# Kernel optimization log

Hardware: AMD Instinct MI355X
Metric: run time of the kernel (lower is better)

Reference implementation:

```python
import jax, jax.numpy as jnp
import numpy as np

DIM = 256
HEADS = 4
DEPTH = DIM // HEADS
EXPAND = 4
EPS = 1e-3  # keras BatchNormalization default epsilon


def _bn(x, gamma, beta, mean, var):
    # inference-mode batch norm over last axis
    return gamma * (x - mean) * jax.lax.rsqrt(var + EPS) + beta


def setup_inputs() -> dict:
    key = jax.random.key(0)
    ks = jax.random.split(key, 12)
    B, S, D = 4, 2048, DIM
    H = D * EXPAND
    s = 1.0 / np.sqrt(D)
    inp = {
        "x": jax.random.normal(ks[0], (B, S, D), jnp.float32),
        "bn1_gamma": jnp.ones((D,), jnp.float32),
        "bn1_beta": jnp.zeros((D,), jnp.float32),
        "bn1_mean": jax.random.normal(ks[1], (D,), jnp.float32) * 0.1,
        "bn1_var": jnp.abs(jax.random.normal(ks[2], (D,), jnp.float32)) + 0.5,
        "wq": jax.random.normal(ks[3], (D, D), jnp.float32) * s,
        "bq": jnp.zeros((D,), jnp.float32),
        "wk": jax.random.normal(ks[4], (D, D), jnp.float32) * s,
        "bk": jnp.zeros((D,), jnp.float32),
        "wv": jax.random.normal(ks[5], (D, D), jnp.float32) * s,
        "bv": jnp.zeros((D,), jnp.float32),
        "wo": jax.random.normal(ks[6], (D, D), jnp.float32) * s,
        "bo": jnp.zeros((D,), jnp.float32),
        "bn2_gamma": jnp.ones((D,), jnp.float32),
        "bn2_beta": jnp.zeros((D,), jnp.float32),
        "bn2_mean": jax.random.normal(ks[7], (D,), jnp.float32) * 0.1,
        "bn2_var": jnp.abs(jax.random.normal(ks[8], (D,), jnp.float32)) + 0.5,
        "w1": jax.random.normal(ks[9], (D, H), jnp.float32) * s,
        "w2": jax.random.normal(ks[10], (H, D), jnp.float32) * (1.0 / np.sqrt(H)),
    }
    return inp


def reference(x, bn1_gamma, bn1_beta, bn1_mean, bn1_var,
              wq, bq, wk, bk, wv, bv, wo, bo,
              bn2_gamma, bn2_beta, bn2_mean, bn2_var, w1, w2):
    B, S, D = x.shape
    h = _bn(x, bn1_gamma, bn1_beta, bn1_mean, bn1_var)
    # project and split heads -> [B, H, S, depth]
    def heads(t):
        return t.reshape(B, S, HEADS, DEPTH).transpose(0, 2, 1, 3)
    q = heads(h @ wq + bq)
    k = heads(h @ wk + bk)
    v = heads(h @ wv + bv)
    scores = jnp.einsum("bhqd,bhkd->bhqk", q, k) / jnp.sqrt(jnp.float32(DEPTH))
    attn = jax.nn.softmax(scores, axis=-1)
    ctx = jnp.einsum("bhqk,bhkd->bhqd", attn, v)
    ctx = ctx.transpose(0, 2, 1, 3).reshape(B, S, D)
    attn_out = ctx @ wo + bo
    x1 = attn_out + x  # residual (dropout = identity at inference)
    h2 = _bn(x1, bn2_gamma, bn2_beta, bn2_mean, bn2_var)
    m = jax.nn.gelu(h2 @ w1, approximate=False) @ w2
    return m + x1
```

## Files before the change

### kernel.cpp

```cpp
#include <hip/hip_runtime.h>

typedef unsigned short u16;
typedef unsigned int u32;
typedef short short8 __attribute__((ext_vector_type(8)));
typedef short short4v __attribute__((ext_vector_type(4)));
typedef float f32x4 __attribute__((ext_vector_type(4)));

#define EPS 1e-3f
#define C1F 0.18033688011112042f

#if defined(__HIP_DEVICE_COMPILE__)
#define MFMA16(a, b, c) __builtin_amdgcn_mfma_f32_16x16x16bf16_1k(a, b, c, 0, 0, 0)
#else
#define MFMA16(a, b, c) (c)
#endif

static __device__ __forceinline__ u16 f2bf(float f) {
    u32 u = __float_as_uint(f);
    u += 0x7fffu + ((u >> 16) & 1u);
    return (u16)(u >> 16);
}
static __device__ __forceinline__ float bf2f(u16 v) {
    u32 u = (u32)v << 16;
    return __uint_as_float(u);
}
static __device__ __forceinline__ u32 pack_bf2(float a, float b) {
    u32 ua = __float_as_uint(a) + 0x8000u;
    u32 ub = __float_as_uint(b) + 0x8000u;
    return __builtin_amdgcn_perm(ub, ua, 0x07060302u);
}
static __device__ __forceinline__ void async_cp16(const void* g, void* l) {
    __builtin_amdgcn_global_load_lds(
        (const __attribute__((address_space(1))) unsigned int*)g,
        (__attribute__((address_space(3))) unsigned int*)l, 16, 0, 0);
}

__global__ void prep_kernel(const float* __restrict__ wq, const float* __restrict__ wk,
                            const float* __restrict__ wv, const float* __restrict__ wo,
                            const float* __restrict__ w1, const float* __restrict__ w2,
                            const float* __restrict__ bq, const float* __restrict__ bk,
                            const float* __restrict__ bv,
                            const float* __restrict__ g1, const float* __restrict__ b1,
                            const float* __restrict__ m1, const float* __restrict__ v1,
                            const float* __restrict__ g2, const float* __restrict__ b2,
                            const float* __restrict__ m2, const float* __restrict__ v2,
                            u16* __restrict__ wqkvT, u16* __restrict__ woT,
                            u16* __restrict__ w1T, u16* __restrict__ w2T,
                            float* __restrict__ bqkv,
                            float* __restrict__ bn1sc, float* __restrict__ bn1sh,
                            float* __restrict__ bn2sc, float* __restrict__ bn2sh) {
    int idx = blockIdx.x * 256 + threadIdx.x;
    if (idx < 196608) {
        int sec = idx >> 16;
        int i = idx & 65535;
        int k = i >> 8, n = i & 255;
        const float* w = sec == 0 ? wq : (sec == 1 ? wk : wv);
        float v = w[i];
        if (sec == 1) v *= C1F;
        wqkvT[(sec * 256 + n) * 256 + k] = f2bf(v);
    } else if (idx < 262144) {
        int i = idx - 196608; int k = i >> 8, n = i & 255;
        woT[n * 256 + k] = f2bf(wo[i]);
    } else if (idx < 524288) {
        int i = idx - 262144; int k = i >> 10, n = i & 1023;
        w1T[n * 256 + k] = f2bf(w1[i]);
    } else if (idx < 786432) {
        int i = idx - 524288; int k = i >> 8, n = i & 255;
        w2T[n * 1024 + k] = f2bf(w2[i]);
    } else if (idx < 787200) {
        int i = idx - 786432;
        bqkv[i] = (i < 256) ? bq[i] : (i < 512 ? bk[i - 256] * C1F : bv[i - 512]);
    } else if (idx < 787456) {
        int i = idx - 787200;
        float sc = g1[i] * rsqrtf(v1[i] + EPS);
        bn1sc[i] = sc; bn1sh[i] = b1[i] - m1[i] * sc;
    } else if (idx < 787712) {
        int i = idx - 787456;
        float sc = g2[i] * rsqrtf(v2[i] + EPS);
        bn2sc[i] = sc; bn2sh[i] = b2[i] - m2[i] * sc;
    }
}

__global__ void bn1_kernel(const float* __restrict__ x, const float* __restrict__ sc,
                           const float* __restrict__ sh, u16* __restrict__ h) {
    int idx = blockIdx.x * 256 + threadIdx.x;
    int base = idx * 4;
    int c = base & 255;
    float4 xv = *(const float4*)(x + base);
    float4 s4 = *(const float4*)(sc + c);
    float4 h4 = *(const float4*)(sh + c);
    ushort4 pk;
    pk.x = f2bf(fmaf(xv.x, s4.x, h4.x));
    pk.y = f2bf(fmaf(xv.y, s4.y, h4.y));
    pk.z = f2bf(fmaf(xv.z, s4.z, h4.z));
    pk.w = f2bf(fmaf(xv.w, s4.w, h4.w));
    *(ushort4*)(h + base) = pk;
}

template <int EPI>
__global__ __launch_bounds__(256) void gemm64(
        const u16* __restrict__ A, const u16* __restrict__ Bt,
        int M, int N, int K,
        const float* __restrict__ bias, const float* __restrict__ resid,
        float* __restrict__ out_f32, u16* __restrict__ out_bf,
        u16* __restrict__ out_vt,
        const float* __restrict__ b2sc, const float* __restrict__ b2sh) {
    __shared__ u16 abuf[2][4096];
    __shared__ u16 bbuf[2][4096];
    const int t = threadIdx.x;
    const int w = t >> 6, lane = t & 63;
    const int l = lane & 15, Q = lane >> 4;
    const int m0 = blockIdx.x * 64;
    const int n0 = blockIdx.y * 64;

    f32x4 acc[4];
#pragma unroll
    for (int nt = 0; nt < 4; ++nt) acc[nt] = (f32x4){0.f, 0.f, 0.f, 0.f};

    auto stage = [&](int k0, int b) {
#pragma unroll
        for (int j = 0; j < 2; ++j) {
            int idx = j * 256 + t;
            int r = idx >> 3, c8 = idx & 7;
            int sc = c8 ^ (r & 7);
            async_cp16(A + (size_t)(m0 + r) * K + k0 + sc * 8, abuf[b] + idx * 8);
        }
#pragma unroll
        for (int j = 0; j < 2; ++j) {
            int idx = j * 256 + t;
            int r = idx >> 3, c8 = idx & 7;
            int sc = c8 ^ (r & 7);
            async_cp16(Bt + (size_t)(n0 + r) * K + k0 + sc * 8, bbuf[b] + idx * 8);
        }
    };

    const int nit = K >> 6;
    stage(0, 0);
    for (int i = 0; i < nit; ++i) {
        __syncthreads();
        if (i + 1 < nit) stage((i + 1) << 6, (i + 1) & 1);
        const u16* ab = abuf[i & 1];
        const u16* bb = bbuf[i & 1];
#pragma unroll
        for (int kd = 0; kd < 2; ++kd) {
            int ar = w * 16 + l;
            short8 afr = *(const short8*)(ab + ar * 64 + (((kd * 4 + Q) ^ (ar & 7))) * 8);
#pragma unroll
            for (int nt = 0; nt < 4; ++nt) {
                int r = nt * 16 + l;
                short8 bfr = *(const short8*)(bb + r * 64 + (((kd * 4 + Q) ^ (r & 7))) * 8);
                acc[nt] = __builtin_amdgcn_mfma_f32_16x16x32_bf16(afr, bfr, acc[nt], 0, 0, 0);
            }
        }
    }

#pragma unroll
    for (int nt = 0; nt < 4; ++nt) {
        int col = n0 + nt * 16 + l;
        int row0 = m0 + w * 16 + Q * 4;
        if (EPI == 0) {
            float b = bias[col];
            if (col < 512) {
#pragma unroll
                for (int r = 0; r < 4; ++r)
                    out_bf[(size_t)(row0 + r) * 512 + col] = f2bf(acc[nt][r] + b);
            } else {
                ushort4 pk;
                pk.x = f2bf(acc[nt][0] + b);
                pk.y = f2bf(acc[nt][1] + b);
                pk.z = f2bf(acc[nt][2] + b);
                pk.w = f2bf(acc[nt][3] + b);
                *(ushort4*)(out_vt + (size_t)(col - 512) * 8192 + row0) = pk;
            }
        } else {
#pragma unroll
            for (int r = 0; r < 4; ++r) {
                int row = row0 + r;
                float val = acc[nt][r];
                size_t oidx = (size_t)row * N + col;
                if (EPI == 1) {
                    val += bias[col] + resid[oidx];
                    out_f32[oidx] = val;
                    out_bf[oidx] = f2bf(fmaf(val, b2sc[col], b2sh[col]));
                } else if (EPI == 2) {
                    float gl = 0.5f * val * (1.f + erff(val * 0.70710678118654752f));
                    out_bf[oidx] = f2bf(gl);
                } else {
                    out_f32[oidx] = val + resid[oidx];
                }
            }
        }
    }
}

static __device__ __forceinline__ void stage_tiles8(const u16* kglob, const u16* vglob,
                                                    u16* kdst, u16* vdst,
                                                    int w, int lane, int kt) {
    const int wp = w & 3;
#pragma unroll
    for (int j = 0; j < 2; ++j) {
        int cw = (wp * 2 + j) * 64 + lane;
        int r = cw >> 3;
        int c = (cw & 7) ^ (r & 7);
        if (w < 4)
            async_cp16(kglob + ((size_t)(kt * 64 + r)) * 512 + c * 8, kdst + (wp * 2 + j) * 512);
        else
            async_cp16(vglob + ((size_t)r) * 8192 + kt * 64 + c * 8, vdst + (wp * 2 + j) * 512);
    }
}

__global__ __launch_bounds__(512) void attn_kernel(const u16* __restrict__ qk,
                                                   const u16* __restrict__ vT,
                                                   u16* __restrict__ opart,
                                                   float* __restrict__ lpart) {
    __shared__ u16 kbuf[2][4096];
    __shared__ u16 vbuf[2][4096];
    const int t = threadIdx.x;
    const int w = t >> 6, lane = t & 63;
    const int l = lane & 15, Q = lane >> 4;
    const int qt = blockIdx.x;
    const int bh = blockIdx.y;
    const int sp = blockIdx.z;
    const int bb = bh >> 2, hd = bh & 3;
    const size_t rowbase = (size_t)bb * 2048;
    const int q0 = qt * 256 + w * 32;

    short8 qf[2][2];
#pragma unroll
    for (int qg = 0; qg < 2; ++qg)
#pragma unroll
        for (int kd = 0; kd < 2; ++kd)
            qf[qg][kd] = *(const short8*)(qk + (rowbase + q0 + qg * 16 + l) * 512
                                          + hd * 64 + kd * 32 + Q * 8);

    f32x4 o[2][4];
#pragma unroll
    for (int qg = 0; qg < 2; ++qg)
#pragma unroll
        for (int dt = 0; dt < 4; ++dt) o[qg][dt] = (f32x4){0.f, 0.f, 0.f, 0.f};
    float lacc[2] = {0.f, 0.f};

    const u16* kglob = qk + (rowbase + sp * 256) * 512 + 256 + hd * 64;
    const u16* vglob = vT + ((size_t)(hd * 64)) * 8192 + rowbase + sp * 256;

    stage_tiles8(kglob, vglob, kbuf[0], vbuf[0], w, lane, 0);

    for (int kt = 0; kt < 4; ++kt) {
        __syncthreads();
        if (kt < 3)
            stage_tiles8(kglob, vglob, kbuf[(kt + 1) & 1], vbuf[(kt + 1) & 1], w, lane, kt + 1);
        const u16* kb = kbuf[kt & 1];
        const u16* vb = vbuf[kt & 1];

        union { u32 u[2]; short4v s4; } pf[2][4];
#pragma unroll
        for (int st = 0; st < 4; ++st) {
            int r = st * 16 + l;
            short8 kf0 = *(const short8*)(kb + r * 64 + ((Q) ^ (r & 7)) * 8);
            short8 kf1 = *(const short8*)(kb + r * 64 + ((4 + Q) ^ (r & 7)) * 8);
#pragma unroll
            for (int qg = 0; qg < 2; ++qg) {
                f32x4 s = (f32x4){0.f, 0.f, 0.f, 0.f};
                s = __builtin_amdgcn_mfma_f32_16x16x32_bf16(kf0, qf[qg][0], s, 0, 0, 0);
                s = __builtin_amdgcn_mfma_f32_16x16x32_bf16(kf1, qf[qg][1], s, 0, 0, 0);
                float p0 = exp2f(fminf(s[0], 100.f));
                float p1 = exp2f(fminf(s[1], 100.f));
                float p2 = exp2f(fminf(s[2], 100.f));
                float p3 = exp2f(fminf(s[3], 100.f));
                lacc[qg] += (p0 + p1) + (p2 + p3);
                pf[qg][st].u[0] = pack_bf2(p0, p1);
                pf[qg][st].u[1] = pack_bf2(p2, p3);
            }
        }

#pragma unroll
        for (int c = 0; c < 4; ++c) {
#pragma unroll
            for (int dt = 0; dt < 4; ++dt) {
                int r = dt * 16 + l;
                int slot = (2 * c + (Q >> 1)) ^ (r & 7);
                short4v vf = *(const short4v*)(vb + r * 64 + slot * 8 + (Q & 1) * 4);
                o[0][dt] = MFMA16(vf, pf[0][c].s4, o[0][dt]);
                o[1][dt] = MFMA16(vf, pf[1][c].s4, o[1][dt]);
            }
        }
    }

#pragma unroll
    for (int qg = 0; qg < 2; ++qg) {
        float v = lacc[qg];
        v += __shfl_xor(v, 16);
        v += __shfl_xor(v, 32);
        lacc[qg] = v;
    }
    u16* ob = opart + (((size_t)sp * 16 + bh) * 2048 + q0) * 64;
#pragma unroll
    for (int qg = 0; qg < 2; ++qg)
#pragma unroll
        for (int dt = 0; dt < 4; ++dt) {
            ushort4 pk;
            pk.x = f2bf(o[qg][dt][0]);
            pk.y = f2bf(o[qg][dt][1]);
            pk.z = f2bf(o[qg][dt][2]);
            pk.w = f2bf(o[qg][dt][3]);
            *(ushort4*)(ob + (size_t)(qg * 16 + l) * 64 + dt * 16 + Q * 4) = pk;
        }
    if (Q == 0) {
        size_t lb = ((size_t)sp * 16 + bh) * 2048 + q0;
        lpart[lb + l] = lacc[0];
        lpart[lb + 16 + l] = lacc[1];
    }
}

__global__ void combine_kernel(const u16* __restrict__ opart,
                               const float* __restrict__ lpart,
                               u16* __restrict__ ctx) {
    int idx = blockIdx.x * 256 + threadIdx.x;
    int e = idx * 4;
    int row = e >> 8, col = e & 255;
    int b = row >> 11, s = row & 2047, h = col >> 6, d = col & 63;
    float a0 = 0.f, a1 = 0.f, a2 = 0.f, a3 = 0.f, lsum = 0.f;
#pragma unroll
    for (int sp = 0; sp < 8; ++sp) {
        size_t pb = (((size_t)sp * 16 + b * 4 + h) * 2048 + s) * 64 + d;
        ushort4 ov = *(const ushort4*)(opart + pb);
        a0 += bf2f(ov.x); a1 += bf2f(ov.y); a2 += bf2f(ov.z); a3 += bf2f(ov.w);
        lsum += lpart[((size_t)sp * 16 + b * 4 + h) * 2048 + s];
    }
    float li = 1.0f / lsum;
    ushort4 pk;
    pk.x = f2bf(a0 * li);
    pk.y = f2bf(a1 * li);
    pk.z = f2bf(a2 * li);
    pk.w = f2bf(a3 * li);
    *(ushort4*)(ctx + e) = pk;
}

extern "C" void kernel_launch(void* const* d_in, const int* in_sizes, int n_in,
                              void* d_out, int out_size, void* d_ws, size_t ws_size,
                              hipStream_t stream) {
    (void)in_sizes; (void)n_in; (void)out_size; (void)ws_size;
    const float* x  = (const float*)d_in[0];
    const float* g1 = (const float*)d_in[1];
    const float* b1 = (const float*)d_in[2];
    const float* m1 = (const float*)d_in[3];
    const float* v1 = (const float*)d_in[4];
    const float* wq = (const float*)d_in[5];
    const float* bq = (const float*)d_in[6];
    const float* wk = (const float*)d_in[7];
    const float* bk = (const float*)d_in[8];
    const float* wv = (const float*)d_in[9];
    const float* bv = (const float*)d_in[10];
    const float* wo = (const float*)d_in[11];
    const float* bo = (const float*)d_in[12];
    const float* g2 = (const float*)d_in[13];
    const float* b2 = (const float*)d_in[14];
    const float* m2 = (const float*)d_in[15];
    const float* v2 = (const float*)d_in[16];
    const float* w1 = (const float*)d_in[17];
    const float* w2 = (const float*)d_in[18];

    char* ws = (char*)d_ws;
    u16*   qkb    = (u16*)(ws + (0ull << 20));
    u16*   vTb    = (u16*)(ws + (8ull << 20));
    u16*   h_buf  = (u16*)(ws + (12ull << 20));
    u16*   ctx    = (u16*)(ws + (16ull << 20));
    float* x1     = (float*)(ws + (20ull << 20));
    u16*   h2     = (u16*)(ws + (28ull << 20));
    u16*   gbuf   = (u16*)(ws + (32ull << 20));
    u16*   opart  = (u16*)(ws + (48ull << 20));
    float* lpart  = (float*)(ws + (80ull << 20));
    u16*   wqkvT  = (u16*)(ws + (81ull << 20));
    u16*   woT    = (u16*)(ws + (82ull << 20));
    u16*   w1T    = (u16*)(ws + (83ull << 20));
    u16*   w2T    = (u16*)(ws + (84ull << 20));
    float* bqkv   = (float*)(ws + (85ull << 20));
    float* bn1sc  = (float*)(ws + (85ull << 20) + 4096);
    float* bn1sh  = (float*)(ws + (85ull << 20) + 8192);
    float* bn2sc  = (float*)(ws + (85ull << 20) + 12288);
    float* bn2sh  = (float*)(ws + (85ull << 20) + 16384);
    float* out    = (float*)d_out;

    prep_kernel<<<3077, 256, 0, stream>>>(wq, wk, wv, wo, w1, w2, bq, bk, bv,
                                          g1, b1, m1, v1, g2, b2, m2, v2,
                                          wqkvT, woT, w1T, w2T, bqkv,
                                          bn1sc, bn1sh, bn2sc, bn2sh);
    bn1_kernel<<<2048, 256, 0, stream>>>(x, bn1sc, bn1sh, h_buf);
    gemm64<0><<<dim3(128, 12), 256, 0, stream>>>(
        h_buf, wqkvT, 8192, 768, 256, bqkv, nullptr, nullptr, qkb, vTb, nullptr, nullptr);
    attn_kernel<<<dim3(8, 16, 8), 512, 0, stream>>>(qkb, vTb, opart, lpart);
    combine_kernel<<<2048, 256, 0, stream>>>(opart, lpart, ctx);
    gemm64<1><<<dim3(128, 4), 256, 0, stream>>>(
        ctx, woT, 8192, 256, 256, bo, x, x1, h2, nullptr, bn2sc, bn2sh);
    gemm64<2><<<dim3(128, 16), 256, 0, stream>>>(
        h2, w1T, 8192, 1024, 256, nullptr, nullptr, nullptr, gbuf, nullptr, nullptr, nullptr);
    gemm64<3><<<dim3(128, 4), 256, 0, stream>>>(
        gbuf, w2T, 8192, 256, 1024, nullptr, x1, out, nullptr, nullptr, nullptr, nullptr);
}
```

Before: 199.7 us.

## Fuse FFN GEMMs, merge BN1 into prep, reshape attention blocks

```diff
diff --git a/kernel.cpp b/kernel.cpp
--- a/kernel.cpp
+++ b/kernel.cpp
@@ -24,10 +24,8 @@
     u32 u = (u32)v << 16;
     return __uint_as_float(u);
 }
-static __device__ __forceinline__ u32 pack_bf2(float a, float b) {
-    u32 ua = __float_as_uint(a) + 0x8000u;
-    u32 ub = __float_as_uint(b) + 0x8000u;
-    return __builtin_amdgcn_perm(ub, ua, 0x07060302u);
+static __device__ __forceinline__ u32 pack_bf2_trunc(float a, float b) {
+    return __builtin_amdgcn_perm(__float_as_uint(b), __float_as_uint(a), 0x07060302u);
 }
 static __device__ __forceinline__ void async_cp16(const void* g, void* l) {
     __builtin_amdgcn_global_load_lds(
@@ -35,7 +33,8 @@
         (__attribute__((address_space(3))) unsigned int*)l, 16, 0, 0);
 }
 
-__global__ void prep_kernel(const float* __restrict__ wq, const float* __restrict__ wk,
+__global__ void prep_bn1_kernel(const float* __restrict__ x,
+                            const float* __restrict__ wq, const float* __restrict__ wk,
                             const float* __restrict__ wv, const float* __restrict__ wo,
                             const float* __restrict__ w1, const float* __restrict__ w2,
                             const float* __restrict__ bq, const float* __restrict__ bk,
@@ -44,12 +43,33 @@
                             const float* __restrict__ m1, const float* __restrict__ v1,
                             const float* __restrict__ g2, const float* __restrict__ b2,
                             const float* __restrict__ m2, const float* __restrict__ v2,
+                            u16* __restrict__ h,
                             u16* __restrict__ wqkvT, u16* __restrict__ woT,
                             u16* __restrict__ w1T, u16* __restrict__ w2T,
                             float* __restrict__ bqkv,
                             float* __restrict__ bn1sc, float* __restrict__ bn1sh,
                             float* __restrict__ bn2sc, float* __restrict__ bn2sh) {
-    int idx = blockIdx.x * 256 + threadIdx.x;
+    int bid = blockIdx.x;
+    if (bid < 2048) {
+        int idx = bid * 256 + threadIdx.x;
+        int base = idx * 4;
+        int c = base & 255;
+        float4 xv = *(const float4*)(x + base);
+        ushort4 pk;
+        {
+            float sc0 = g1[c] * rsqrtf(v1[c] + EPS);
+            pk.x = f2bf(fmaf(xv.x, sc0, b1[c] - m1[c] * sc0));
+            float sc1 = g1[c+1] * rsqrtf(v1[c+1] + EPS);
+            pk.y = f2bf(fmaf(xv.y, sc1, b1[c+1] - m1[c+1] * sc1));
+            float sc2 = g1[c+2] * rsqrtf(v1[c+2] + EPS);
+            pk.z = f2bf(fmaf(xv.z, sc2, b1[c+2] - m1[c+2] * sc2));
+            float sc3 = g1[c+3] * rsqrtf(v1[c+3] + EPS);
+            pk.w = f2bf(fmaf(xv.w, sc3, b1[c+3] - m1[c+3] * sc3));
+        }
+        *(ushort4*)(h + base) = pk;
+        return;
+    }
+    int idx = (bid - 2048) * 256 + threadIdx.x;
     if (idx < 196608) {
         int sec = idx >> 16;
         int i = idx & 65535;
@@ -81,22 +101,6 @@
     }
 }
 
-__global__ void bn1_kernel(const float* __restrict__ x, const float* __restrict__ sc,
-                           const float* __restrict__ sh, u16* __restrict__ h) {
-    int idx = blockIdx.x * 256 + threadIdx.x;
-    int base = idx * 4;
-    int c = base & 255;
-    float4 xv = *(const float4*)(x + base);
-    float4 s4 = *(const float4*)(sc + c);
-    float4 h4 = *(const float4*)(sh + c);
-    ushort4 pk;
-    pk.x = f2bf(fmaf(xv.x, s4.x, h4.x));
-    pk.y = f2bf(fmaf(xv.y, s4.y, h4.y));
-    pk.z = f2bf(fmaf(xv.z, s4.z, h4.z));
-    pk.w = f2bf(fmaf(xv.w, s4.w, h4.w));
-    *(ushort4*)(h + base) = pk;
-}
-
 template <int EPI>
 __global__ __launch_bounds__(256) void gemm64(
         const u16* __restrict__ A, const u16* __restrict__ Bt,
@@ -178,43 +182,164 @@
                 int row = row0 + r;
                 float val = acc[nt][r];
                 size_t oidx = (size_t)row * N + col;
-                if (EPI == 1) {
-                    val += bias[col] + resid[oidx];
-                    out_f32[oidx] = val;
-                    out_bf[oidx] = f2bf(fmaf(val, b2sc[col], b2sh[col]));
-                } else if (EPI == 2) {
-                    float gl = 0.5f * val * (1.f + erff(val * 0.70710678118654752f));
-                    out_bf[oidx] = f2bf(gl);
-                } else {
-                    out_f32[oidx] = val + resid[oidx];
-                }
-            }
-        }
-    }
-}
-
-static __device__ __forceinline__ void stage_tiles8(const u16* kglob, const u16* vglob,
-                                                    u16* kdst, u16* vdst,
-                                                    int w, int lane, int kt) {
-    const int wp = w & 3;
+                val += bias[col] + resid[oidx];
+                out_f32[oidx] = val;
+                out_bf[oidx] = f2bf(fmaf(val, b2sc[col], b2sh[col]));
+            }
+        }
+    }
+}
+
+__global__ __launch_bounds__(256) void ffn_fused(
+        const u16* __restrict__ h2, const u16* __restrict__ w1T,
+        const u16* __restrict__ w2T, const float* __restrict__ x1,
+        float* __restrict__ out) {
+    __shared__ u16 h2t[32 * 256];
+    __shared__ u16 gl[32 * 1024];
+    __shared__ u16 wbuf[2][64 * 256];
+    const int t = threadIdx.x;
+    const int w = t >> 6, lane = t & 63;
+    const int l = lane & 15, Q = lane >> 4;
+    const int m0 = blockIdx.x * 32;
+
+#pragma unroll
+    for (int j = 0; j < 4; ++j) {
+        int idx = j * 256 + t;
+        int r = idx >> 5, c = idx & 31;
+        int sc = (c & 24) | ((c & 7) ^ (r & 7));
+        async_cp16(h2 + (size_t)(m0 + r) * 256 + sc * 8, h2t + idx * 8);
+    }
+#pragma unroll
+    for (int j = 0; j < 8; ++j) {
+        int idx = j * 256 + t;
+        int r = idx >> 5, c = idx & 31;
+        int sc = (c & 24) | ((c & 7) ^ (r & 7));
+        async_cp16(w1T + (size_t)r * 256 + sc * 8, wbuf[0] + idx * 8);
+    }
+
+    for (int c0 = 0; c0 < 16; ++c0) {
+        __syncthreads();
+        if (c0 < 15) {
+#pragma unroll
+            for (int j = 0; j < 8; ++j) {
+                int idx = j * 256 + t;
+                int r = idx >> 5, c = idx & 31;
+                int sc = (c & 24) | ((c & 7) ^ (r & 7));
+                async_cp16(w1T + (size_t)((c0 + 1) * 64 + r) * 256 + sc * 8,
+                           wbuf[(c0 + 1) & 1] + idx * 8);
+            }
+        } else {
+#pragma unroll
+            for (int j = 0; j < 8; ++j) {
+                int idx = j * 256 + t;
+                int r = idx >> 3, c = idx & 7;
+                int sc = c ^ (r & 7);
+                async_cp16(w2T + (size_t)r * 1024 + sc * 8, wbuf[0] + idx * 8);
+            }
+        }
+        const u16* wb = wbuf[c0 & 1];
+        f32x4 acc[2];
+        acc[0] = (f32x4){0.f, 0.f, 0.f, 0.f};
+        acc[1] = (f32x4){0.f, 0.f, 0.f, 0.f};
+#pragma unroll
+        for (int kd = 0; kd < 8; ++kd) {
+            int ch = kd * 4 + Q;
+            int rB = w * 16 + l;
+            short8 bfr = *(const short8*)(wb + rB * 256 + ((ch & 24) | ((ch & 7) ^ (rB & 7))) * 8);
+#pragma unroll
+            for (int mt = 0; mt < 2; ++mt) {
+                int rA = mt * 16 + l;
+                short8 afr = *(const short8*)(h2t + rA * 256 + ((ch & 24) | ((ch & 7) ^ (rA & 7))) * 8);
+                acc[mt] = __builtin_amdgcn_mfma_f32_16x16x32_bf16(afr, bfr, acc[mt], 0, 0, 0);
+            }
+        }
+#pragma unroll
+        for (int mt = 0; mt < 2; ++mt)
+#pragma unroll
+            for (int r = 0; r < 4; ++r) {
+                int row = mt * 16 + Q * 4 + r;
+                int k = c0 * 64 + w * 16 + l;
+                float v = acc[mt][r];
+                float g = 0.5f * v * (1.f + erff(v * 0.70710678118654752f));
+                int chunki = k >> 3;
+                int swz = (chunki & ~7) | ((chunki & 7) ^ (row & 7));
+                gl[row * 1024 + swz * 8 + (k & 7)] = f2bf(g);
+            }
+    }
+
+    f32x4 acc2[2][4];
+#pragma unroll
+    for (int mt = 0; mt < 2; ++mt)
+#pragma unroll
+        for (int nt = 0; nt < 4; ++nt) acc2[mt][nt] = (f32x4){0.f, 0.f, 0.f, 0.f};
+
+    for (int c2 = 0; c2 < 16; ++c2) {
+        __syncthreads();
+        if (c2 < 15) {
+#pragma unroll
+            for (int j = 0; j < 8; ++j) {
+                int idx = j * 256 + t;
+                int r = idx >> 3, c = idx & 7;
+                int sc = c ^ (r & 7);
+                async_cp16(w2T + (size_t)r * 1024 + (c2 + 1) * 64 + sc * 8,
+                           wbuf[(c2 + 1) & 1] + idx * 8);
+            }
+        }
+        const u16* wb = wbuf[c2 & 1];
+#pragma unroll
+        for (int kd = 0; kd < 2; ++kd) {
+            short8 afr[2];
+#pragma unroll
+            for (int mt = 0; mt < 2; ++mt) {
+                int rA = mt * 16 + l;
+                int chunki = c2 * 8 + kd * 4 + Q;
+                int swz = (chunki & ~7) | ((chunki & 7) ^ (rA & 7));
+                afr[mt] = *(const short8*)(gl + rA * 1024 + swz * 8);
+            }
+#pragma unroll
+            for (int nt = 0; nt < 4; ++nt) {
+                int rB = w * 64 + nt * 16 + l;
+                int ch = kd * 4 + Q;
+                short8 bfr = *(const short8*)(wb + rB * 64 + (ch ^ (rB & 7)) * 8);
+#pragma unroll
+                for (int mt = 0; mt < 2; ++mt)
+                    acc2[mt][nt] = __builtin_amdgcn_mfma_f32_16x16x32_bf16(afr[mt], bfr, acc2[mt][nt], 0, 0, 0);
+            }
+        }
+    }
+
+#pragma unroll
+    for (int mt = 0; mt < 2; ++mt)
+#pragma unroll
+        for (int nt = 0; nt < 4; ++nt)
+#pragma unroll
+            for (int r = 0; r < 4; ++r) {
+                int row = m0 + mt * 16 + Q * 4 + r;
+                int col = w * 64 + nt * 16 + l;
+                size_t oidx = (size_t)row * 256 + col;
+                out[oidx] = acc2[mt][nt][r] + x1[oidx];
+            }
+}
+
+static __device__ __forceinline__ void stage_tiles(const u16* kglob, const u16* vglob,
+                                                   u16* kdst, u16* vdst,
+                                                   int w, int lane, int kt) {
 #pragma unroll
     for (int j = 0; j < 2; ++j) {
-        int cw = (wp * 2 + j) * 64 + lane;
+        int cw = (w * 2 + j) * 64 + lane;
         int r = cw >> 3;
         int c = (cw & 7) ^ (r & 7);
-        if (w < 4)
-            async_cp16(kglob + ((size_t)(kt * 64 + r)) * 512 + c * 8, kdst + (wp * 2 + j) * 512);
-        else
-            async_cp16(vglob + ((size_t)r) * 8192 + kt * 64 + c * 8, vdst + (wp * 2 + j) * 512);
-    }
-}
-
-__global__ __launch_bounds__(512) void attn_kernel(const u16* __restrict__ qk,
+        async_cp16(kglob + ((size_t)(kt * 64 + r)) * 512 + c * 8, kdst + (w * 2 + j) * 512);
+        async_cp16(vglob + ((size_t)r) * 8192 + kt * 64 + c * 8, vdst + (w * 2 + j) * 512);
+    }
+}
+
+__global__ __launch_bounds__(256) void attn_kernel(const u16* __restrict__ qk,
                                                    const u16* __restrict__ vT,
                                                    u16* __restrict__ opart,
                                                    float* __restrict__ lpart) {
-    __shared__ u16 kbuf[2][4096];
-    __shared__ u16 vbuf[2][4096];
+    __shared__ u16 kbuf[4096];
+    __shared__ u16 vbuf[4096];
     const int t = threadIdx.x;
     const int w = t >> 6, lane = t & 63;
     const int l = lane & 15, Q = lane >> 4;
@@ -223,7 +348,7 @@
     const int sp = blockIdx.z;
     const int bb = bh >> 2, hd = bh & 3;
     const size_t rowbase = (size_t)bb * 2048;
-    const int q0 = qt * 256 + w * 32;
+    const int q0 = qt * 128 + w * 32;
 
     short8 qf[2][2];
 #pragma unroll
@@ -243,33 +368,28 @@
     const u16* kglob = qk + (rowbase + sp * 256) * 512 + 256 + hd * 64;
     const u16* vglob = vT + ((size_t)(hd * 64)) * 8192 + rowbase + sp * 256;
 
-    stage_tiles8(kglob, vglob, kbuf[0], vbuf[0], w, lane, 0);
-
     for (int kt = 0; kt < 4; ++kt) {
+        stage_tiles(kglob, vglob, kbuf, vbuf, w, lane, kt);
         __syncthreads();
-        if (kt < 3)
-            stage_tiles8(kglob, vglob, kbuf[(kt + 1) & 1], vbuf[(kt + 1) & 1], w, lane, kt + 1);
-        const u16* kb = kbuf[kt & 1];
-        const u16* vb = vbuf[kt & 1];
 
         union { u32 u[2]; short4v s4; } pf[2][4];
 #pragma unroll
         for (int st = 0; st < 4; ++st) {
             int r = st * 16 + l;
-            short8 kf0 = *(const short8*)(kb + r * 64 + ((Q) ^ (r & 7)) * 8);
-            short8 kf1 = *(const short8*)(kb + r * 64 + ((4 + Q) ^ (r & 7)) * 8);
+            short8 kf0 = *(const short8*)(kbuf + r * 64 + ((Q) ^ (r & 7)) * 8);
+            short8 kf1 = *(const short8*)(kbuf + r * 64 + ((4 + Q) ^ (r & 7)) * 8);
 #pragma unroll
             for (int qg = 0; qg < 2; ++qg) {
                 f32x4 s = (f32x4){0.f, 0.f, 0.f, 0.f};
                 s = __builtin_amdgcn_mfma_f32_16x16x32_bf16(kf0, qf[qg][0], s, 0, 0, 0);
                 s = __builtin_amdgcn_mfma_f32_16x16x32_bf16(kf1, qf[qg][1], s, 0, 0, 0);
-                float p0 = exp2f(fminf(s[0], 100.f));
-                float p1 = exp2f(fminf(s[1], 100.f));
-                float p2 = exp2f(fminf(s[2], 100.f));
-                float p3 = exp2f(fminf(s[3], 100.f));
+                float p0 = exp2f(s[0]);
+                float p1 = exp2f(s[1]);
+                float p2 = exp2f(s[2]);
+                float p3 = exp2f(s[3]);
                 lacc[qg] += (p0 + p1) + (p2 + p3);
-                pf[qg][st].u[0] = pack_bf2(p0, p1);
-                pf[qg][st].u[1] = pack_bf2(p2, p3);
+                pf[qg][st].u[0] = pack_bf2_trunc(p0, p1);
+                pf[qg][st].u[1] = pack_bf2_trunc(p2, p3);
             }
         }
 
@@ -279,11 +399,12 @@
             for (int dt = 0; dt < 4; ++dt) {
                 int r = dt * 16 + l;
                 int slot = (2 * c + (Q >> 1)) ^ (r & 7);
-                short4v vf = *(const short4v*)(vb + r * 64 + slot * 8 + (Q & 1) * 4);
+                short4v vf = *(const short4v*)(vbuf + r * 64 + slot * 8 + (Q & 1) * 4);
                 o[0][dt] = MFMA16(vf, pf[0][c].s4, o[0][dt]);
                 o[1][dt] = MFMA16(vf, pf[1][c].s4, o[1][dt]);
             }
         }
+        __syncthreads();
     }
 
 #pragma unroll
@@ -367,7 +488,6 @@
     u16*   ctx    = (u16*)(ws + (16ull << 20));
     float* x1     = (float*)(ws + (20ull << 20));
     u16*   h2     = (u16*)(ws + (28ull << 20));
-    u16*   gbuf   = (u16*)(ws + (32ull << 20));
     u16*   opart  = (u16*)(ws + (48ull << 20));
     float* lpart  = (float*)(ws + (80ull << 20));
     u16*   wqkvT  = (u16*)(ws + (81ull << 20));
@@ -381,19 +501,15 @@
     float* bn2sh  = (float*)(ws + (85ull << 20) + 16384);
     float* out    = (float*)d_out;
 
-    prep_kernel<<<3077, 256, 0, stream>>>(wq, wk, wv, wo, w1, w2, bq, bk, bv,
-                                          g1, b1, m1, v1, g2, b2, m2, v2,
-                                          wqkvT, woT, w1T, w2T, bqkv,
-                                          bn1sc, bn1sh, bn2sc, bn2sh);
-    bn1_kernel<<<2048, 256, 0, stream>>>(x, bn1sc, bn1sh, h_buf);
+    prep_bn1_kernel<<<5125, 256, 0, stream>>>(x, wq, wk, wv, wo, w1, w2, bq, bk, bv,
+                                              g1, b1, m1, v1, g2, b2, m2, v2,
+                                              h_buf, wqkvT, woT, w1T, w2T, bqkv,
+                                              bn1sc, bn1sh, bn2sc, bn2sh);
     gemm64<0><<<dim3(128, 12), 256, 0, stream>>>(
         h_buf, wqkvT, 8192, 768, 256, bqkv, nullptr, nullptr, qkb, vTb, nullptr, nullptr);
-    attn_kernel<<<dim3(8, 16, 8), 512, 0, stream>>>(qkb, vTb, opart, lpart);
+    attn_kernel<<<dim3(16, 16, 8), 256, 0, stream>>>(qkb, vTb, opart, lpart);
     combine_kernel<<<2048, 256, 0, stream>>>(opart, lpart, ctx);
     gemm64<1><<<dim3(128, 4), 256, 0, stream>>>(
         ctx, woT, 8192, 256, 256, bo, x, x1, h2, nullptr, bn2sc, bn2sh);
-    gemm64<2><<<dim3(128, 16), 256, 0, stream>>>(
-        h2, w1T, 8192, 1024, 256, nullptr, nullptr, nullptr, gbuf, nullptr, nullptr, nullptr);
-    gemm64<3><<<dim3(128, 4), 256, 0, stream>>>(
-        gbuf, w2T, 8192, 256, 1024, nullptr, x1, out, nullptr, nullptr, nullptr, nullptr);
-}
+    ffn_fused<<<256, 256, 0, stream>>>(h2, w1T, w2T, x1, out);
+}
```

Result: no change. 202.4 us (+1.3%).

## Fuse bn1 into prep kernel and shrink attention blocks to single-buffered 256 threads

Applied to the files above, without the earlier changes.

```diff
diff --git a/kernel.cpp b/kernel.cpp
--- a/kernel.cpp
+++ b/kernel.cpp
@@ -24,10 +24,8 @@
     u32 u = (u32)v << 16;
     return __uint_as_float(u);
 }
-static __device__ __forceinline__ u32 pack_bf2(float a, float b) {
-    u32 ua = __float_as_uint(a) + 0x8000u;
-    u32 ub = __float_as_uint(b) + 0x8000u;
-    return __builtin_amdgcn_perm(ub, ua, 0x07060302u);
+static __device__ __forceinline__ u32 pack_bf2_trunc(float a, float b) {
+    return __builtin_amdgcn_perm(__float_as_uint(b), __float_as_uint(a), 0x07060302u);
 }
 static __device__ __forceinline__ void async_cp16(const void* g, void* l) {
     __builtin_amdgcn_global_load_lds(
@@ -35,7 +33,8 @@
         (__attribute__((address_space(3))) unsigned int*)l, 16, 0, 0);
 }
 
-__global__ void prep_kernel(const float* __restrict__ wq, const float* __restrict__ wk,
+__global__ void prep_bn1_kernel(const float* __restrict__ x,
+                            const float* __restrict__ wq, const float* __restrict__ wk,
                             const float* __restrict__ wv, const float* __restrict__ wo,
                             const float* __restrict__ w1, const float* __restrict__ w2,
                             const float* __restrict__ bq, const float* __restrict__ bk,
@@ -44,12 +43,32 @@
                             const float* __restrict__ m1, const float* __restrict__ v1,
                             const float* __restrict__ g2, const float* __restrict__ b2,
                             const float* __restrict__ m2, const float* __restrict__ v2,
+                            u16* __restrict__ h,
                             u16* __restrict__ wqkvT, u16* __restrict__ woT,
                             u16* __restrict__ w1T, u16* __restrict__ w2T,
                             float* __restrict__ bqkv,
-                            float* __restrict__ bn1sc, float* __restrict__ bn1sh,
                             float* __restrict__ bn2sc, float* __restrict__ bn2sh) {
-    int idx = blockIdx.x * 256 + threadIdx.x;
+    int bid = blockIdx.x;
+    if (bid < 2048) {
+        int idx = bid * 256 + threadIdx.x;
+        int base = idx * 4;
+        int c = base & 255;
+        float4 xv = *(const float4*)(x + base);
+        ushort4 pk;
+        {
+            float sc0 = g1[c] * rsqrtf(v1[c] + EPS);
+            pk.x = f2bf(fmaf(xv.x, sc0, b1[c] - m1[c] * sc0));
+            float sc1 = g1[c+1] * rsqrtf(v1[c+1] + EPS);
+            pk.y = f2bf(fmaf(xv.y, sc1, b1[c+1] - m1[c+1] * sc1));
+            float sc2 = g1[c+2] * rsqrtf(v1[c+2] + EPS);
+            pk.z = f2bf(fmaf(xv.z, sc2, b1[c+2] - m1[c+2] * sc2));
+            float sc3 = g1[c+3] * rsqrtf(v1[c+3] + EPS);
+            pk.w = f2bf(fmaf(xv.w, sc3, b1[c+3] - m1[c+3] * sc3));
+        }
+        *(ushort4*)(h + base) = pk;
+        return;
+    }
+    int idx = (bid - 2048) * 256 + threadIdx.x;
     if (idx < 196608) {
         int sec = idx >> 16;
         int i = idx & 65535;
@@ -72,29 +91,9 @@
         bqkv[i] = (i < 256) ? bq[i] : (i < 512 ? bk[i - 256] * C1F : bv[i - 512]);
     } else if (idx < 787456) {
         int i = idx - 787200;
-        float sc = g1[i] * rsqrtf(v1[i] + EPS);
-        bn1sc[i] = sc; bn1sh[i] = b1[i] - m1[i] * sc;
-    } else if (idx < 787712) {
-        int i = idx - 787456;
         float sc = g2[i] * rsqrtf(v2[i] + EPS);
         bn2sc[i] = sc; bn2sh[i] = b2[i] - m2[i] * sc;
     }
-}
-
-__global__ void bn1_kernel(const float* __restrict__ x, const float* __restrict__ sc,
-                           const float* __restrict__ sh, u16* __restrict__ h) {
-    int idx = blockIdx.x * 256 + threadIdx.x;
-    int base = idx * 4;
-    int c = base & 255;
-    float4 xv = *(const float4*)(x + base);
-    float4 s4 = *(const float4*)(sc + c);
-    float4 h4 = *(const float4*)(sh + c);
-    ushort4 pk;
-    pk.x = f2bf(fmaf(xv.x, s4.x, h4.x));
-    pk.y = f2bf(fmaf(xv.y, s4.y, h4.y));
-    pk.z = f2bf(fmaf(xv.z, s4.z, h4.z));
-    pk.w = f2bf(fmaf(xv.w, s4.w, h4.w));
-    *(ushort4*)(h + base) = pk;
 }
 
 template <int EPI>
@@ -193,28 +192,25 @@
     }
 }
 
-static __device__ __forceinline__ void stage_tiles8(const u16* kglob, const u16* vglob,
-                                                    u16* kdst, u16* vdst,
-                                                    int w, int lane, int kt) {
-    const int wp = w & 3;
+static __device__ __forceinline__ void stage_tiles(const u16* kglob, const u16* vglob,
+                                                   u16* kdst, u16* vdst,
+                                                   int w, int lane, int kt) {
 #pragma unroll
     for (int j = 0; j < 2; ++j) {
-        int cw = (wp * 2 + j) * 64 + lane;
+        int cw = (w * 2 + j) * 64 + lane;
         int r = cw >> 3;
         int c = (cw & 7) ^ (r & 7);
-        if (w < 4)
-            async_cp16(kglob + ((size_t)(kt * 64 + r)) * 512 + c * 8, kdst + (wp * 2 + j) * 512);
-        else
-            async_cp16(vglob + ((size_t)r) * 8192 + kt * 64 + c * 8, vdst + (wp * 2 + j) * 512);
-    }
-}
-
-__global__ __launch_bounds__(512) void attn_kernel(const u16* __restrict__ qk,
+        async_cp16(kglob + ((size_t)(kt * 64 + r)) * 512 + c * 8, kdst + (w * 2 + j) * 512);
+        async_cp16(vglob + ((size_t)r) * 8192 + kt * 64 + c * 8, vdst + (w * 2 + j) * 512);
+    }
+}
+
+__global__ __launch_bounds__(256) void attn_kernel(const u16* __restrict__ qk,
                                                    const u16* __restrict__ vT,
                                                    u16* __restrict__ opart,
                                                    float* __restrict__ lpart) {
-    __shared__ u16 kbuf[2][4096];
-    __shared__ u16 vbuf[2][4096];
+    __shared__ u16 kbuf[4096];
+    __shared__ u16 vbuf[4096];
     const int t = threadIdx.x;
     const int w = t >> 6, lane = t & 63;
     const int l = lane & 15, Q = lane >> 4;
@@ -223,7 +219,7 @@
     const int sp = blockIdx.z;
     const int bb = bh >> 2, hd = bh & 3;
     const size_t rowbase = (size_t)bb * 2048;
-    const int q0 = qt * 256 + w * 32;
+    const int q0 = qt * 128 + w * 32;
 
     short8 qf[2][2];
 #pragma unroll
@@ -243,33 +239,28 @@
     const u16* kglob = qk + (rowbase + sp * 256) * 512 + 256 + hd * 64;
     const u16* vglob = vT + ((size_t)(hd * 64)) * 8192 + rowbase + sp * 256;
 
-    stage_tiles8(kglob, vglob, kbuf[0], vbuf[0], w, lane, 0);
-
     for (int kt = 0; kt < 4; ++kt) {
+        stage_tiles(kglob, vglob, kbuf, vbuf, w, lane, kt);
         __syncthreads();
-        if (kt < 3)
-            stage_tiles8(kglob, vglob, kbuf[(kt + 1) & 1], vbuf[(kt + 1) & 1], w, lane, kt + 1);
-        const u16* kb = kbuf[kt & 1];
-        const u16* vb = vbuf[kt & 1];
 
         union { u32 u[2]; short4v s4; } pf[2][4];
 #pragma unroll
         for (int st = 0; st < 4; ++st) {
             int r = st * 16 + l;
-            short8 kf0 = *(const short8*)(kb + r * 64 + ((Q) ^ (r & 7)) * 8);
-            short8 kf1 = *(const short8*)(kb + r * 64 + ((4 + Q) ^ (r & 7)) * 8);
+            short8 kf0 = *(const short8*)(kbuf + r * 64 + ((Q) ^ (r & 7)) * 8);
+            short8 kf1 = *(const short8*)(kbuf + r * 64 + ((4 + Q) ^ (r & 7)) * 8);
 #pragma unroll
             for (int qg = 0; qg < 2; ++qg) {
                 f32x4 s = (f32x4){0.f, 0.f, 0.f, 0.f};
                 s = __builtin_amdgcn_mfma_f32_16x16x32_bf16(kf0, qf[qg][0], s, 0, 0, 0);
                 s = __builtin_amdgcn_mfma_f32_16x16x32_bf16(kf1, qf[qg][1], s, 0, 0, 0);
-                float p0 = exp2f(fminf(s[0], 100.f));
-                float p1 = exp2f(fminf(s[1], 100.f));
-                float p2 = exp2f(fminf(s[2], 100.f));
-                float p3 = exp2f(fminf(s[3], 100.f));
+                float p0 = exp2f(s[0]);
+                float p1 = exp2f(s[1]);
+                float p2 = exp2f(s[2]);
+                float p3 = exp2f(s[3]);
                 lacc[qg] += (p0 + p1) + (p2 + p3);
-                pf[qg][st].u[0] = pack_bf2(p0, p1);
-                pf[qg][st].u[1] = pack_bf2(p2, p3);
+                pf[qg][st].u[0] = pack_bf2_trunc(p0, p1);
+                pf[qg][st].u[1] = pack_bf2_trunc(p2, p3);
             }
         }
 
@@ -279,11 +270,12 @@
             for (int dt = 0; dt < 4; ++dt) {
                 int r = dt * 16 + l;
                 int slot = (2 * c + (Q >> 1)) ^ (r & 7);
-                short4v vf = *(const short4v*)(vb + r * 64 + slot * 8 + (Q & 1) * 4);
+                short4v vf = *(const short4v*)(vbuf + r * 64 + slot * 8 + (Q & 1) * 4);
                 o[0][dt] = MFMA16(vf, pf[0][c].s4, o[0][dt]);
                 o[1][dt] = MFMA16(vf, pf[1][c].s4, o[1][dt]);
             }
         }
+        __syncthreads();
     }
 
 #pragma unroll
@@ -375,20 +367,17 @@
     u16*   w1T    = (u16*)(ws + (83ull << 20));
     u16*   w2T    = (u16*)(ws + (84ull << 20));
     float* bqkv   = (float*)(ws + (85ull << 20));
-    float* bn1sc  = (float*)(ws + (85ull << 20) + 4096);
-    float* bn1sh  = (float*)(ws + (85ull << 20) + 8192);
-    float* bn2sc  = (float*)(ws + (85ull << 20) + 12288);
-    float* bn2sh  = (float*)(ws + (85ull << 20) + 16384);
+    float* bn2sc  = (float*)(ws + (85ull << 20) + 4096);
+    float* bn2sh  = (float*)(ws + (85ull << 20) + 8192);
     float* out    = (float*)d_out;
 
-    prep_kernel<<<3077, 256, 0, stream>>>(wq, wk, wv, wo, w1, w2, bq, bk, bv,
-                                          g1, b1, m1, v1, g2, b2, m2, v2,
-                                          wqkvT, woT, w1T, w2T, bqkv,
-                                          bn1sc, bn1sh, bn2sc, bn2sh);
-    bn1_kernel<<<2048, 256, 0, stream>>>(x, bn1sc, bn1sh, h_buf);
+    prep_bn1_kernel<<<5125, 256, 0, stream>>>(x, wq, wk, wv, wo, w1, w2, bq, bk, bv,
+                                              g1, b1, m1, v1, g2, b2, m2, v2,
+                                              h_buf, wqkvT, woT, w1T, w2T, bqkv,
+                                              bn2sc, bn2sh);
     gemm64<0><<<dim3(128, 12), 256, 0, stream>>>(
         h_buf, wqkvT, 8192, 768, 256, bqkv, nullptr, nullptr, qkb, vTb, nullptr, nullptr);
-    attn_kernel<<<dim3(8, 16, 8), 512, 0, stream>>>(qkb, vTb, opart, lpart);
+    attn_kernel<<<dim3(16, 16, 8), 256, 0, stream>>>(qkb, vTb, opart, lpart);
     combine_kernel<<<2048, 256, 0, stream>>>(opart, lpart, ctx);
     gemm64<1><<<dim3(128, 4), 256, 0, stream>>>(
         ctx, woT, 8192, 256, 256, bo, x, x1, h2, nullptr, bn2sc, bn2sh);
```

Result: faster. 187.7 us (-6.0%).
